# Kernel tuning notes

Hardware: AMD Instinct MI355X
Metric: run time of the kernel (lower is better)

The kernel has to match this reference:

```python
import jax, jax.numpy as jnp
import numpy as np

EPS = 1e-6
HEADS = 8
DIM_HEAD = 64
SCALE = 16.0
DIM = 1024
INNER = HEADS * DIM_HEAD


def _l2norm(t):
    return t / jnp.clip(jnp.linalg.norm(t, axis=-1, keepdims=True), 1e-12)


def setup_inputs() -> dict:
    key = jax.random.key(0)
    k1, k2, k3, k4 = jax.random.split(key, 4)
    b, n = 2, 4096
    x = jax.random.normal(k1, (b, n, DIM), dtype=jnp.float32)
    # weights stored as [in, out] so application is x @ W
    Wq = jax.random.normal(k2, (DIM, INNER), dtype=jnp.float32) * 0.02
    Wkv = jax.random.normal(k3, (DIM, 2 * INNER), dtype=jnp.float32) * 0.02
    Wo = jax.random.normal(k4, (INNER, DIM), dtype=jnp.float32) * 0.02
    return {"x": x, "Wq": Wq, "Wkv": Wkv, "Wo": Wo}


def reference(x, Wq, Wkv, Wo):
    b, n, _ = x.shape
    q = (x @ Wq).reshape(b, n, HEADS, DIM_HEAD).transpose(0, 2, 1, 3)  # b h n d
    kv = x @ Wkv
    k = kv[..., :INNER].reshape(b, n, HEADS, DIM_HEAD).transpose(0, 2, 1, 3)
    v = kv[..., INNER:].reshape(b, n, HEADS, DIM_HEAD).transpose(0, 2, 1, 3)
    q = _l2norm(q)
    k = _l2norm(k)
    # cosine-sim attention: logits = scale * (q.k) - scale, logits <= 0 so exp is stable
    logits = jnp.einsum('bhid,bhjd->bhij', q, k) * SCALE - SCALE
    p = jnp.exp(logits)
    row_sums = jnp.clip(p.sum(axis=-1, keepdims=True), EPS)  # matches per-block EPS clamp in dense case
    out = jnp.einsum('bhij,bhjd->bhid', p, v) / row_sums  # b h n d
    out = out.transpose(0, 2, 1, 3).reshape(b, n, INNER)
    return out @ Wo
```

## Files before the change

kernel.cpp:

```cpp
#include <hip/hip_runtime.h>


typedef _Float16 f16;
typedef _Float16 f16x4 __attribute__((ext_vector_type(4)));
typedef _Float16 f16x8 __attribute__((ext_vector_type(8)));
typedef float f32x4 __attribute__((ext_vector_type(4)));

#define MFMA_F16(a, b, c) __builtin_amdgcn_mfma_f32_16x16x32_f16((a), (b), (c), 0, 0, 0)

__device__ __forceinline__ void gl_lds16(const void* g, void* l) {
  __builtin_amdgcn_global_load_lds(
      (const __attribute__((address_space(1))) void*)g,
      (__attribute__((address_space(3))) void*)l, 16, 0, 0);
}

__global__ void convert_x_kernel(const float* __restrict__ x, f16* __restrict__ xh, int n8) {
  int i = blockIdx.x * 256 + threadIdx.x;
  if (i >= n8) return;
  const float4* xv = (const float4*)x;
  float4 a = xv[2 * i], b = xv[2 * i + 1];
  f16x8 o;
  o[0] = (f16)a.x; o[1] = (f16)a.y; o[2] = (f16)a.z; o[3] = (f16)a.w;
  o[4] = (f16)b.x; o[5] = (f16)b.y; o[6] = (f16)b.z; o[7] = (f16)b.w;
  ((f16x8*)xh)[i] = o;
}

__global__ void transpose_w_kernel(const float* __restrict__ W, int ldw, int col0,
                                   int K, f16* __restrict__ out) {
  __shared__ float t[64][65];
  int tx = threadIdx.x, ty = threadIdx.y;
  int c0 = blockIdx.x * 64, k0 = blockIdx.y * 64;
#pragma unroll
  for (int i = 0; i < 8; i++)
    t[ty + i * 8][tx] = W[(long)(k0 + ty + i * 8) * ldw + col0 + c0 + tx];
  __syncthreads();
#pragma unroll
  for (int i = 0; i < 8; i++)
    out[(long)(c0 + ty + i * 8) * K + k0 + tx] = (f16)t[tx][ty + i * 8];
}

__global__ void transpose_v_kernel(const f16* __restrict__ Vb, f16* __restrict__ Vt, int n) {
  __shared__ f16 t[64 * 64];
  const int tid = threadIdx.x;
  const int bh = blockIdx.y;
  const int n0 = blockIdx.x * 64;
  const f16* src = Vb + ((long)bh * n + n0) * 64;
  const int j = tid >> 3, c = tid & 7;
  f16x8 v0 = *(const f16x8*)(src + j * 64 + c * 8);
  f16x8 v1 = *(const f16x8*)(src + (j + 32) * 64 + c * 8);
  *(f16x8*)(&t[j * 64 + ((c ^ (j & 7)) << 3)]) = v0;
  *(f16x8*)(&t[(j + 32) * 64 + ((c ^ (j & 7)) << 3)]) = v1;
  __syncthreads();
  const int d = tid >> 3, cj = tid & 7;
  f16x8 o0, o1;
#pragma unroll
  for (int e = 0; e < 8; e++) {
    int jj = cj * 8 + e;
    o0[e] = t[jj * 64 + (((d >> 3) ^ (jj & 7)) << 3) + (d & 7)];
    o1[e] = t[jj * 64 + ((((d + 32) >> 3) ^ (jj & 7)) << 3) + ((d + 32) & 7)];
  }
  *(f16x8*)(Vt + ((long)bh * 64 + d) * n + n0 + cj * 8) = o0;
  *(f16x8*)(Vt + ((long)bh * 64 + d + 32) * n + n0 + cj * 8) = o1;
}

template <int MODE>
__global__ __launch_bounds__(256, 2)
void gemm_kernel(const f16* __restrict__ A, const f16* __restrict__ Bt,
                 float* __restrict__ C,
                 f16* __restrict__ Qb, f16* __restrict__ Kb, f16* __restrict__ Vb,
                 int M, int N, int K) {
  __shared__ f16 As[128 * 32];
  __shared__ f16 Bs[128 * 32];
  const int tid = threadIdx.x;
  const int lane = tid & 63;
  const int wid = tid >> 6;
  const int wr = wid >> 1, wc = wid & 1;
  const int lr = lane & 15, lk = lane >> 4;
  const long m0 = (long)blockIdx.x * 128;
  const int n0 = blockIdx.y * 128;

  f32x4 acc[4][4] = {};

  const int c0 = tid, c1 = tid + 256;
  const int ar0 = c0 >> 2, ah0 = (c0 & 3) ^ ((ar0 >> 1) & 3);
  const int ar1 = c1 >> 2, ah1 = (c1 & 3) ^ ((ar1 >> 1) & 3);
  const f16* pa0 = A + (m0 + ar0) * K + ah0 * 8;
  const f16* pa1 = A + (m0 + ar1) * K + ah1 * 8;
  const f16* pb0 = Bt + (long)(n0 + ar0) * K + ah0 * 8;
  const f16* pb1 = Bt + (long)(n0 + ar1) * K + ah1 * 8;

  for (int k0 = 0; k0 < K; k0 += 32) {
    __syncthreads();
    gl_lds16(pa0 + k0, As + c0 * 8);
    gl_lds16(pa1 + k0, As + c1 * 8);
    gl_lds16(pb0 + k0, Bs + c0 * 8);
    gl_lds16(pb1 + k0, Bs + c1 * 8);
    __syncthreads();

    f16x8 af[4], bf[4];
#pragma unroll
    for (int mi = 0; mi < 4; mi++) {
      int row = wr * 64 + mi * 16 + lr;
      int ch = lk ^ ((row >> 1) & 3);
      af[mi] = *(const f16x8*)(As + row * 32 + ch * 8);
    }
#pragma unroll
    for (int ni = 0; ni < 4; ni++) {
      int row = wc * 64 + ni * 16 + lr;
      int ch = lk ^ ((row >> 1) & 3);
      bf[ni] = *(const f16x8*)(Bs + row * 32 + ch * 8);
    }
#pragma unroll
    for (int mi = 0; mi < 4; mi++)
#pragma unroll
      for (int ni = 0; ni < 4; ni++)
        acc[mi][ni] = MFMA_F16(af[mi], bf[ni], acc[mi][ni]);
  }

  if (MODE == 0) {
#pragma unroll
    for (int mi = 0; mi < 4; mi++) {
      long mrow = m0 + wr * 64 + mi * 16 + lk * 4;
#pragma unroll
      for (int r = 0; r < 4; r++)
#pragma unroll
        for (int ni = 0; ni < 4; ni++)
          C[(mrow + r) * N + n0 + wc * 64 + ni * 16 + lr] = acc[mi][ni][r];
    }
  } else {
    const int region = blockIdx.y >> 2;
    const int head = (blockIdx.y & 3) * 2 + wc;
    f16* buf = (region == 0) ? Qb : ((region == 1) ? Kb : Vb);
#pragma unroll
    for (int mi = 0; mi < 4; mi++) {
      float scl[4];
      if (region < 2) {
#pragma unroll
        for (int r = 0; r < 4; r++) {
          float s2 = 0.f;
#pragma unroll
          for (int ni = 0; ni < 4; ni++) s2 += acc[mi][ni][r] * acc[mi][ni][r];
          s2 += __shfl_xor(s2, 1);
          s2 += __shfl_xor(s2, 2);
          s2 += __shfl_xor(s2, 4);
          s2 += __shfl_xor(s2, 8);
          scl[r] = 1.f / fmaxf(sqrtf(s2), 1e-12f);
        }
      } else {
#pragma unroll
        for (int r = 0; r < 4; r++) scl[r] = 1.f;
      }
#pragma unroll
      for (int r = 0; r < 4; r++) {
        int m = (int)m0 + wr * 64 + mi * 16 + lk * 4 + r;
        int bb = m >> 12, nn = m & 4095;
        f16* dst = buf + (((long)(bb * 8 + head) * 4096 + nn) << 6);
#pragma unroll
        for (int ni = 0; ni < 4; ni++)
          dst[ni * 16 + lr] = (f16)(acc[mi][ni][r] * scl[r]);
      }
    }
  }
}

__global__ __launch_bounds__(512, 2)
void attn_kernel(const f16* __restrict__ Qb, const f16* __restrict__ Kb,
                 const f16* __restrict__ Vt, f16* __restrict__ Ob, int n) {
  __shared__ f16 Ks[2][64 * 64];
  __shared__ f16 Vs[2][64 * 64];
  __shared__ f16 Ps[8][16 * 64];
  const int tid = threadIdx.x, lane = tid & 63, wid = tid >> 6;
  const int lr = lane & 15, lk = lane >> 4;
  const int bh = blockIdx.y;
  const long nl = n;
  const f16* Qg = Qb + (long)bh * nl * 64;
  const f16* Kg = Kb + (long)bh * nl * 64;
  const f16* Vg = Vt + (long)bh * 64 * nl;
  const int q0 = blockIdx.x * 128 + wid * 16;

  f16x8 qf[2];
#pragma unroll
  for (int kc = 0; kc < 2; kc++)
    qf[kc] = *(const f16x8*)(Qg + (long)(q0 + lr) * 64 + kc * 32 + lk * 8);

  const int sr = tid >> 3;
  const int sc = (tid & 7) ^ (sr & 7);

  f32x4 oacc[4] = {};
  float rsum = 0.f;

  gl_lds16(Kg + (long)sr * 64 + sc * 8, &Ks[0][tid * 8]);
  gl_lds16(Vg + (long)sr * nl + sc * 8, &Vs[0][tid * 8]);
  __syncthreads();

  const int nt = n >> 6;
  for (int t = 0; t < nt; t++) {
    const int cur = t & 1;
    if (t + 1 < nt) {
      const long j0 = (long)(t + 1) << 6;
      gl_lds16(Kg + (j0 + sr) * 64 + sc * 8, &Ks[cur ^ 1][tid * 8]);
      gl_lds16(Vg + (long)sr * nl + j0 + sc * 8, &Vs[cur ^ 1][tid * 8]);
    }

    f32x4 s[4] = {};
#pragma unroll
    for (int kc = 0; kc < 2; kc++)
#pragma unroll
      for (int jt = 0; jt < 4; jt++) {
        const int j = jt * 16 + lr;
        const f16x8 kf =
            *(const f16x8*)(&Ks[cur][j * 64 + (((kc * 4 + lk) ^ (j & 7)) << 3)]);
        s[jt] = MFMA_F16(kf, qf[kc], s[jt]);
      }

#pragma unroll
    for (int jt = 0; jt < 4; jt++) {
      const f32x4 sv = s[jt];
      const float p0 = __builtin_amdgcn_exp2f(fmaf(sv[0], 23.083120654223414f, -9.083120654223414f));
      const float p1 = __builtin_amdgcn_exp2f(fmaf(sv[1], 23.083120654223414f, -9.083120654223414f));
      const float p2 = __builtin_amdgcn_exp2f(fmaf(sv[2], 23.083120654223414f, -9.083120654223414f));
      const float p3 = __builtin_amdgcn_exp2f(fmaf(sv[3], 23.083120654223414f, -9.083120654223414f));
      rsum += (p0 + p1) + (p2 + p3);
      const auto h01 = __builtin_amdgcn_cvt_pkrtz(p0, p1);
      const auto h23 = __builtin_amdgcn_cvt_pkrtz(p2, p3);
      f16x4 pk;
      pk[0] = h01[0]; pk[1] = h01[1]; pk[2] = h23[0]; pk[3] = h23[1];
      const int c16 = jt * 2 + (lk >> 1);
      *(f16x4*)(&Ps[wid][lr * 64 + ((c16 ^ (lr & 7)) << 3) + ((lk & 1) << 2)]) = pk;
    }

#pragma unroll
    for (int kc = 0; kc < 2; kc++) {
      const int c16 = kc * 4 + lk;
      const f16x8 pa = *(const f16x8*)(&Ps[wid][lr * 64 + ((c16 ^ (lr & 7)) << 3)]);
      f16x8 vf[4];
#pragma unroll
      for (int dt = 0; dt < 4; dt++) {
        const int d = dt * 16 + lr;
        vf[dt] = *(const f16x8*)(&Vs[cur][d * 64 + ((c16 ^ (d & 7)) << 3)]);
      }
#pragma unroll
      for (int dt = 0; dt < 4; dt++)
        oacc[dt] = MFMA_F16(pa, vf[dt], oacc[dt]);
    }

    __syncthreads();
  }

  rsum += __shfl_xor(rsum, 16);
  rsum += __shfl_xor(rsum, 32);
  const int bb = bh >> 3, hh = bh & 7;
#pragma unroll
  for (int r = 0; r < 4; r++) {
    const float sm = __shfl(rsum, lk * 4 + r);
    const float inv = 1.f / fmaxf(sm, 0.016384f);
    const int qq = q0 + lk * 4 + r;
    f16* dst = Ob + (((long)(bb * 4096 + qq)) << 9) + hh * 64;
#pragma unroll
    for (int dt = 0; dt < 4; dt++)
      dst[dt * 16 + lr] = (f16)(oacc[dt][r] * inv);
  }
}

extern "C" void kernel_launch(void* const* d_in, const int* in_sizes, int n_in,
                              void* d_out, int out_size, void* d_ws, size_t ws_size,
                              hipStream_t stream) {
  const float* x   = (const float*)d_in[0];
  const float* Wq  = (const float*)d_in[1];
  const float* Wkv = (const float*)d_in[2];
  const float* Wo  = (const float*)d_in[3];
  float* out = (float*)d_out;

  char* ws = (char*)d_ws;
  f16* xh     = (f16*)(ws);
  f16* Wqkv_t = (f16*)(ws + 16777216);
  f16* Wo_t   = (f16*)(ws + 19922944);
  f16* Qb     = (f16*)(ws + 20971520);
  f16* Kb     = (f16*)(ws + 29360128);
  f16* Vb     = (f16*)(ws + 37748736);
  f16* At     = (f16*)(ws + 46137344);
  f16* Vt     = xh;

  convert_x_kernel<<<4096, 256, 0, stream>>>(x, xh, 1048576);

  dim3 tb(64, 8);
  transpose_w_kernel<<<dim3(8, 16), tb, 0, stream>>>(Wq, 512, 0, 1024, Wqkv_t);
  transpose_w_kernel<<<dim3(8, 16), tb, 0, stream>>>(Wkv, 1024, 0, 1024, Wqkv_t + 512 * 1024);
  transpose_w_kernel<<<dim3(8, 16), tb, 0, stream>>>(Wkv, 1024, 512, 1024, Wqkv_t + 1024 * 1024);
  transpose_w_kernel<<<dim3(16, 8), tb, 0, stream>>>(Wo, 1024, 0, 512, Wo_t);

  gemm_kernel<1><<<dim3(64, 12), 256, 0, stream>>>(xh, Wqkv_t, nullptr, Qb, Kb, Vb,
                                                   8192, 1536, 1024);
  transpose_v_kernel<<<dim3(64, 16), 256, 0, stream>>>(Vb, Vt, 4096);
  attn_kernel<<<dim3(32, 16), 512, 0, stream>>>(Qb, Kb, Vt, At, 4096);
  gemm_kernel<0><<<dim3(64, 8), 256, 0, stream>>>(At, Wo_t, out, nullptr, nullptr, nullptr,
                                                  8192, 1024, 512);
}
```

Measured before the change: 173.8 us.

## Remap block order for XCD locality, enlarge attention KV tiles, add MFMA priority hints

Both GEMM launches and the attention kernel move to a 1D grid whose block index is swizzled, so neighbouring blocks (likely placed on the same XCD) share operand tiles or the same head in L2. The attention kernel doubles its K/V tile to 128 keys per iteration, halving the loop trips and barriers, and splits the P·V step into two sub-chunks. It also raises the occupancy hint to 4 and wraps MFMA sections in s_setprio. The larger LDS footprint and extra live score registers may limit how many blocks fit per CU and could cause register spills.

```diff
diff --git a/kernel.cpp b/kernel.cpp
--- a/kernel.cpp
+++ b/kernel.cpp
@@ -76,8 +76,11 @@
   const int wid = tid >> 6;
   const int wr = wid >> 1, wc = wid & 1;
   const int lr = lane & 15, lk = lane >> 4;
-  const long m0 = (long)blockIdx.x * 128;
-  const int n0 = blockIdx.y * 128;
+  const int lin = blockIdx.x;
+  const int bx = ((lin & 7) << 3) | ((lin >> 3) & 7);
+  const int by = lin >> 6;
+  const long m0 = (long)bx * 128;
+  const int n0 = by * 128;
 
   f32x4 acc[4][4] = {};
 
@@ -110,11 +113,13 @@
       int ch = lk ^ ((row >> 1) & 3);
       bf[ni] = *(const f16x8*)(Bs + row * 32 + ch * 8);
     }
+    __builtin_amdgcn_s_setprio(1);
 #pragma unroll
     for (int mi = 0; mi < 4; mi++)
 #pragma unroll
       for (int ni = 0; ni < 4; ni++)
         acc[mi][ni] = MFMA_F16(af[mi], bf[ni], acc[mi][ni]);
+    __builtin_amdgcn_s_setprio(0);
   }
 
   if (MODE == 0) {
@@ -128,8 +133,8 @@
           C[(mrow + r) * N + n0 + wc * 64 + ni * 16 + lr] = acc[mi][ni][r];
     }
   } else {
-    const int region = blockIdx.y >> 2;
-    const int head = (blockIdx.y & 3) * 2 + wc;
+    const int region = by >> 2;
+    const int head = (by & 3) * 2 + wc;
     f16* buf = (region == 0) ? Qb : ((region == 1) ? Kb : Vb);
 #pragma unroll
     for (int mi = 0; mi < 4; mi++) {
@@ -163,85 +168,100 @@
   }
 }
 
-__global__ __launch_bounds__(512, 2)
+__global__ __launch_bounds__(512, 4)
 void attn_kernel(const f16* __restrict__ Qb, const f16* __restrict__ Kb,
                  const f16* __restrict__ Vt, f16* __restrict__ Ob, int n) {
-  __shared__ f16 Ks[2][64 * 64];
-  __shared__ f16 Vs[2][64 * 64];
+  __shared__ f16 Ks[2][128 * 64];
+  __shared__ f16 Vs[2][64 * 128];
   __shared__ f16 Ps[8][16 * 64];
   const int tid = threadIdx.x, lane = tid & 63, wid = tid >> 6;
   const int lr = lane & 15, lk = lane >> 4;
-  const int bh = blockIdx.y;
+  const int lin = blockIdx.x;
+  const int bh = (lin & 7) | ((lin >> 8) << 3);
+  const int qx = (lin >> 3) & 31;
   const long nl = n;
   const f16* Qg = Qb + (long)bh * nl * 64;
   const f16* Kg = Kb + (long)bh * nl * 64;
   const f16* Vg = Vt + (long)bh * 64 * nl;
-  const int q0 = blockIdx.x * 128 + wid * 16;
+  const int q0 = qx * 128 + wid * 16;
 
   f16x8 qf[2];
 #pragma unroll
   for (int kc = 0; kc < 2; kc++)
     qf[kc] = *(const f16x8*)(Qg + (long)(q0 + lr) * 64 + kc * 32 + lk * 8);
 
-  const int sr = tid >> 3;
-  const int sc = (tid & 7) ^ (sr & 7);
+  const int krow = tid >> 3;
+  const int kcol = ((tid & 7) ^ (krow & 7)) * 8;
+  const int vrow = tid >> 4;
+  const int vcol = ((tid & 15) ^ (vrow & 15)) * 8;
 
   f32x4 oacc[4] = {};
   float rsum = 0.f;
-
-  gl_lds16(Kg + (long)sr * 64 + sc * 8, &Ks[0][tid * 8]);
-  gl_lds16(Vg + (long)sr * nl + sc * 8, &Vs[0][tid * 8]);
+  const f32x4 zero4 = {0.f, 0.f, 0.f, 0.f};
+
+  gl_lds16(Kg + (long)krow * 64 + kcol, &Ks[0][tid * 8]);
+  gl_lds16(Kg + (long)(krow + 64) * 64 + kcol, &Ks[0][tid * 8 + 4096]);
+  gl_lds16(Vg + (long)vrow * nl + vcol, &Vs[0][tid * 8]);
+  gl_lds16(Vg + (long)(vrow + 32) * nl + vcol, &Vs[0][tid * 8 + 4096]);
   __syncthreads();
 
-  const int nt = n >> 6;
+  const int nt = n >> 7;
   for (int t = 0; t < nt; t++) {
     const int cur = t & 1;
     if (t + 1 < nt) {
-      const long j0 = (long)(t + 1) << 6;
-      gl_lds16(Kg + (j0 + sr) * 64 + sc * 8, &Ks[cur ^ 1][tid * 8]);
-      gl_lds16(Vg + (long)sr * nl + j0 + sc * 8, &Vs[cur ^ 1][tid * 8]);
-    }
-
-    f32x4 s[4] = {};
-#pragma unroll
-    for (int kc = 0; kc < 2; kc++)
-#pragma unroll
-      for (int jt = 0; jt < 4; jt++) {
-        const int j = jt * 16 + lr;
-        const f16x8 kf =
-            *(const f16x8*)(&Ks[cur][j * 64 + (((kc * 4 + lk) ^ (j & 7)) << 3)]);
-        s[jt] = MFMA_F16(kf, qf[kc], s[jt]);
+      const long j0 = (long)(t + 1) << 7;
+      gl_lds16(Kg + (j0 + krow) * 64 + kcol, &Ks[cur ^ 1][tid * 8]);
+      gl_lds16(Kg + (j0 + krow + 64) * 64 + kcol, &Ks[cur ^ 1][tid * 8 + 4096]);
+      gl_lds16(Vg + (long)vrow * nl + j0 + vcol, &Vs[cur ^ 1][tid * 8]);
+      gl_lds16(Vg + (long)(vrow + 32) * nl + j0 + vcol, &Vs[cur ^ 1][tid * 8 + 4096]);
+    }
+
+    f32x4 s[8];
+    __builtin_amdgcn_s_setprio(1);
+#pragma unroll
+    for (int jt = 0; jt < 8; jt++) {
+      const int j = jt * 16 + lr;
+      const f16x8 kf0 = *(const f16x8*)(&Ks[cur][j * 64 + ((lk ^ (j & 7)) << 3)]);
+      const f16x8 kf1 = *(const f16x8*)(&Ks[cur][j * 64 + (((4 + lk) ^ (j & 7)) << 3)]);
+      f32x4 acc0 = MFMA_F16(kf0, qf[0], zero4);
+      s[jt] = MFMA_F16(kf1, qf[1], acc0);
+    }
+    __builtin_amdgcn_s_setprio(0);
+
+#pragma unroll
+    for (int sub = 0; sub < 2; sub++) {
+#pragma unroll
+      for (int jt2 = 0; jt2 < 4; jt2++) {
+        const f32x4 sv = s[sub * 4 + jt2];
+        const float p0 = __builtin_amdgcn_exp2f(fmaf(sv[0], 23.083120654223414f, -9.083120654223414f));
+        const float p1 = __builtin_amdgcn_exp2f(fmaf(sv[1], 23.083120654223414f, -9.083120654223414f));
+        const float p2 = __builtin_amdgcn_exp2f(fmaf(sv[2], 23.083120654223414f, -9.083120654223414f));
+        const float p3 = __builtin_amdgcn_exp2f(fmaf(sv[3], 23.083120654223414f, -9.083120654223414f));
+        rsum += (p0 + p1) + (p2 + p3);
+        const auto h01 = __builtin_amdgcn_cvt_pkrtz(p0, p1);
+        const auto h23 = __builtin_amdgcn_cvt_pkrtz(p2, p3);
+        f16x4 pk;
+        pk[0] = h01[0]; pk[1] = h01[1]; pk[2] = h23[0]; pk[3] = h23[1];
+        const int c16 = jt2 * 2 + (lk >> 1);
+        *(f16x4*)(&Ps[wid][lr * 64 + ((c16 ^ (lr & 7)) << 3) + ((lk & 1) << 2)]) = pk;
       }
 
-#pragma unroll
-    for (int jt = 0; jt < 4; jt++) {
-      const f32x4 sv = s[jt];
-      const float p0 = __builtin_amdgcn_exp2f(fmaf(sv[0], 23.083120654223414f, -9.083120654223414f));
-      const float p1 = __builtin_amdgcn_exp2f(fmaf(sv[1], 23.083120654223414f, -9.083120654223414f));
-      const float p2 = __builtin_amdgcn_exp2f(fmaf(sv[2], 23.083120654223414f, -9.083120654223414f));
-      const float p3 = __builtin_amdgcn_exp2f(fmaf(sv[3], 23.083120654223414f, -9.083120654223414f));
-      rsum += (p0 + p1) + (p2 + p3);
-      const auto h01 = __builtin_amdgcn_cvt_pkrtz(p0, p1);
-      const auto h23 = __builtin_amdgcn_cvt_pkrtz(p2, p3);
-      f16x4 pk;
-      pk[0] = h01[0]; pk[1] = h01[1]; pk[2] = h23[0]; pk[3] = h23[1];
-      const int c16 = jt * 2 + (lk >> 1);
-      *(f16x4*)(&Ps[wid][lr * 64 + ((c16 ^ (lr & 7)) << 3) + ((lk & 1) << 2)]) = pk;
-    }
-
-#pragma unroll
-    for (int kc = 0; kc < 2; kc++) {
-      const int c16 = kc * 4 + lk;
-      const f16x8 pa = *(const f16x8*)(&Ps[wid][lr * 64 + ((c16 ^ (lr & 7)) << 3)]);
-      f16x8 vf[4];
-#pragma unroll
-      for (int dt = 0; dt < 4; dt++) {
-        const int d = dt * 16 + lr;
-        vf[dt] = *(const f16x8*)(&Vs[cur][d * 64 + ((c16 ^ (d & 7)) << 3)]);
+      __builtin_amdgcn_s_setprio(1);
+#pragma unroll
+      for (int kc2 = 0; kc2 < 2; kc2++) {
+        const int c16 = kc2 * 4 + lk;
+        const f16x8 pa = *(const f16x8*)(&Ps[wid][lr * 64 + ((c16 ^ (lr & 7)) << 3)]);
+        f16x8 vf[4];
+#pragma unroll
+        for (int dt = 0; dt < 4; dt++) {
+          const int d = dt * 16 + lr;
+          vf[dt] = *(const f16x8*)(&Vs[cur][d * 128 + (((sub * 8 + kc2 * 4 + lk) ^ (d & 15)) << 3)]);
+        }
+#pragma unroll
+        for (int dt = 0; dt < 4; dt++)
+          oacc[dt] = MFMA_F16(pa, vf[dt], oacc[dt]);
       }
-#pragma unroll
-      for (int dt = 0; dt < 4; dt++)
-        oacc[dt] = MFMA_F16(pa, vf[dt], oacc[dt]);
+      __builtin_amdgcn_s_setprio(0);
     }
 
     __syncthreads();
@@ -289,10 +309,10 @@
   transpose_w_kernel<<<dim3(8, 16), tb, 0, stream>>>(Wkv, 1024, 512, 1024, Wqkv_t + 1024 * 1024);
   transpose_w_kernel<<<dim3(16, 8), tb, 0, stream>>>(Wo, 1024, 0, 512, Wo_t);
 
-  gemm_kernel<1><<<dim3(64, 12), 256, 0, stream>>>(xh, Wqkv_t, nullptr, Qb, Kb, Vb,
-                                                   8192, 1536, 1024);
+  gemm_kernel<1><<<768, 256, 0, stream>>>(xh, Wqkv_t, nullptr, Qb, Kb, Vb,
+                                          8192, 1536, 1024);
   transpose_v_kernel<<<dim3(64, 16), 256, 0, stream>>>(Vb, Vt, 4096);
-  attn_kernel<<<dim3(32, 16), 512, 0, stream>>>(Qb, Kb, Vt, At, 4096);
-  gemm_kernel<0><<<dim3(64, 8), 256, 0, stream>>>(At, Wo_t, out, nullptr, nullptr, nullptr,
-                                                  8192, 1024, 512);
-}
+  attn_kernel<<<512, 512, 0, stream>>>(Qb, Kb, Vt, At, 4096);
+  gemm_kernel<0><<<512, 256, 0, stream>>>(At, Wo_t, out, nullptr, nullptr, nullptr,
+                                          8192, 1024, 512);
+}
```

After: 170.2 us. 1.02x faster.
